# Performance work log

Hardware: AMD Instinct MI355X
Metric: run time of the kernel (lower is better)

Reference implementation:

```python
import jax, jax.numpy as jnp
import numpy as np

EMB = 768
N_HEADS = 12
HEAD_DIM = EMB // N_HEADS
EPS = 1e-5


def _gelu_tanh(x):
    c = jnp.sqrt(jnp.asarray(2.0 / jnp.pi, x.dtype))
    return 0.5 * x * (1.0 + jnp.tanh(c * (x + 0.044715 * x ** 3)))


def _layernorm(x, scale, shift):
    mean = jnp.mean(x, axis=-1, keepdims=True)
    var = jnp.mean((x - mean) ** 2, axis=-1, keepdims=True)
    return (x - mean) / jnp.sqrt(var + EPS) * scale + shift


def setup_inputs() -> dict:
    key = jax.random.key(0)
    ks = jax.random.split(key, 8)
    s = 0.02  # GPT-2 style init scale
    x = jax.random.normal(ks[0], (8, 1024, EMB), dtype=jnp.float32)
    # torch Linear weights are (out, in); no biases (qkv_bias=False everywhere)
    wq = jax.random.normal(ks[1], (EMB, EMB), dtype=jnp.float32) * s
    wk = jax.random.normal(ks[2], (EMB, EMB), dtype=jnp.float32) * s
    wv = jax.random.normal(ks[3], (EMB, EMB), dtype=jnp.float32) * s
    wo = jax.random.normal(ks[4], (EMB, EMB), dtype=jnp.float32) * s
    w1 = jax.random.normal(ks[5], (4 * EMB, EMB), dtype=jnp.float32) * s
    w2 = jax.random.normal(ks[6], (EMB, 4 * EMB), dtype=jnp.float32) * s
    ln1_scale = jnp.ones((EMB,), jnp.float32)
    ln1_shift = jnp.zeros((EMB,), jnp.float32)
    ln2_scale = jnp.ones((EMB,), jnp.float32)
    ln2_shift = jnp.zeros((EMB,), jnp.float32)
    return dict(x=x, wq=wq, wk=wk, wv=wv, wo=wo, w1=w1, w2=w2,
                ln1_scale=ln1_scale, ln1_shift=ln1_shift,
                ln2_scale=ln2_scale, ln2_shift=ln2_shift)


def reference(x, wq, wk, wv, wo, w1, w2, ln1_scale, ln1_shift, ln2_scale, ln2_shift):
    B, T, E = x.shape
    # --- attention sublayer (pre-LN) ---
    h = _layernorm(x, ln1_scale, ln1_shift)
    q = (h @ wq.T).reshape(B, T, N_HEADS, HEAD_DIM).transpose(0, 2, 1, 3)
    k = (h @ wk.T).reshape(B, T, N_HEADS, HEAD_DIM).transpose(0, 2, 1, 3)
    v = (h @ wv.T).reshape(B, T, N_HEADS, HEAD_DIM).transpose(0, 2, 1, 3)
    scores = jnp.einsum('bhqd,bhkd->bhqk', q, k)  # [B,H,T,T]
    causal = jnp.tril(jnp.ones((T, T), dtype=bool))
    scores = jnp.where(causal, scores, -jnp.inf)
    attn = jax.nn.softmax(scores / np.sqrt(HEAD_DIM), axis=-1)
    ctx = jnp.einsum('bhqk,bhkd->bhqd', attn, v)
    ctx = ctx.transpose(0, 2, 1, 3).reshape(B, T, E)
    x = x + ctx @ wo.T
    # --- FFN sublayer (pre-LN) ---
    h = _layernorm(x, ln2_scale, ln2_shift)
    h = _gelu_tanh(h @ w1.T) @ w2.T
    return x + h
```

## Files before the change

kernel.cpp:

```cpp
#include <hip/hip_runtime.h>
#include <hip/hip_bf16.h>
#include <cstdint>

#define EMB    768
#define NHEADS 12
#define HDIM   64
#define SEQ    1024
#define BATCH  8
#define MROWS  (BATCH*SEQ)
#define FFN    3072
#define W2E    (EMB*EMB)
#define W4E    (FFN*EMB)

typedef __bf16 bf16_t;
typedef bf16_t bf16x8 __attribute__((ext_vector_type(8)));
typedef float  f32x4  __attribute__((ext_vector_type(4)));

__device__ __forceinline__ float b2f(unsigned short u) {
    union { unsigned int i; float f; } t; t.i = ((unsigned int)u) << 16; return t.f;
}
__device__ __forceinline__ unsigned short f2b(float f) {
    union { float f; unsigned int i; } t; t.f = f;
    unsigned int lsb = (t.i >> 16) & 1u;
    t.i += 0x7fffu + lsb;
    return (unsigned short)(t.i >> 16);
}
__device__ __forceinline__ float gelu_f(float x) {
    float u = 0.7978845608028654f * (x + 0.044715f * x * x * x);
    return x * (1.f / (1.f + __expf(-2.f * u)));
}

#if defined(__has_builtin)
#if __has_builtin(__builtin_amdgcn_global_load_lds)
#define HAS_GLL 1
#endif
#endif
#ifndef HAS_GLL
#define HAS_GLL 0
#endif

__device__ __forceinline__ void gll16(const unsigned short* g, unsigned short* lds_wave_base) {
#if HAS_GLL
    __builtin_amdgcn_global_load_lds(
        (const __attribute__((address_space(1))) unsigned int*)g,
        (__attribute__((address_space(3))) unsigned int*)lds_wave_base, 16, 0, 0);
#endif
}

__device__ __forceinline__ int4 load8(const void* src, size_t eoff, bool f32) {
    if (f32) {
        const float4* p = reinterpret_cast<const float4*>((const float*)src + eoff);
        float4 a = p[0], b = p[1];
        union { unsigned short u[8]; int4 v; } r;
        r.u[0] = f2b(a.x); r.u[1] = f2b(a.y); r.u[2] = f2b(a.z); r.u[3] = f2b(a.w);
        r.u[4] = f2b(b.x); r.u[5] = f2b(b.y); r.u[6] = f2b(b.z); r.u[7] = f2b(b.w);
        return r.v;
    }
    return *reinterpret_cast<const int4*>((const unsigned short*)src + eoff);
}
__device__ __forceinline__ float4 load4f(const void* src, size_t eoff, bool f32) {
    if (f32) return *reinterpret_cast<const float4*>((const float*)src + eoff);
    ushort4 u = *reinterpret_cast<const ushort4*>((const unsigned short*)src + eoff);
    float4 r; r.x = b2f(u.x); r.y = b2f(u.y); r.z = b2f(u.z); r.w = b2f(u.w);
    return r;
}

struct DetectArgs { const unsigned short* p[11]; int n[11]; };

__global__ __launch_bounds__(256) void detect_all(DetectArgs a, int* __restrict__ flags) {
    __shared__ int cnt;
    if (threadIdx.x == 0) cnt = 0;
    __syncthreads();
    const unsigned short* src = a.p[blockIdx.x];
    int npairs = a.n[blockIdx.x] / 2;
    if (npairs > 4096) npairs = 4096;
    int local = 0;
    for (int p = threadIdx.x; p < npairs; p += 256) {
        unsigned short u0 = src[2 * p], u1 = src[2 * p + 1];
        int e0 = (u0 >> 7) & 0xFF;
        bool insane0 = (e0 == 0xFF) || (u0 != 0 && (e0 < 96 || e0 > 159));
        bool zpat    = (u0 == 0 && u1 != 0);
        if (insane0 || zpat) ++local;
    }
    atomicAdd(&cnt, local);
    __syncthreads();
    if (threadIdx.x == 0) flags[blockIdx.x] = (cnt * 8 > npairs) ? 1 : 0;
}

__global__ __launch_bounds__(256) void cvt_adapt(
        const void* __restrict__ src, unsigned short* __restrict__ dst,
        int n, const int* __restrict__ flag) {
    int i = blockIdx.x * 256 + threadIdx.x;
    if (i * 4 >= n) return;
    if (*flag) {
        float4 f = reinterpret_cast<const float4*>(src)[i];
        ushort4 o;
        o.x = f2b(f.x); o.y = f2b(f.y); o.z = f2b(f.z); o.w = f2b(f.w);
        reinterpret_cast<ushort4*>(dst)[i] = o;
    } else {
        reinterpret_cast<ushort4*>(dst)[i] = reinterpret_cast<const ushort4*>(src)[i];
    }
}

struct CvtArgs {
    const void* src[6];
    unsigned short* dst[6];
    int n[6];
    int blkoff[7];
    const int* F;
    int fidx[6];
};
__global__ __launch_bounds__(256) void cvt_weights(CvtArgs a) {
    int b = blockIdx.x, seg = 0;
    #pragma unroll
    for (int s = 0; s < 6; ++s) if (b >= a.blkoff[s + 1]) seg = s + 1;
    int i = (b - a.blkoff[seg]) * 256 + threadIdx.x;
    if (i * 4 >= a.n[seg]) return;
    if (a.F[a.fidx[seg]]) {
        float4 f = reinterpret_cast<const float4*>(a.src[seg])[i];
        ushort4 o;
        o.x = f2b(f.x); o.y = f2b(f.y); o.z = f2b(f.z); o.w = f2b(f.w);
        reinterpret_cast<ushort4*>(a.dst[seg])[i] = o;
    } else {
        reinterpret_cast<ushort4*>(a.dst[seg])[i] =
            reinterpret_cast<const ushort4*>(a.src[seg])[i];
    }
}

__global__ __launch_bounds__(256) void reduce2_kernel(
        const float* __restrict__ P, const unsigned short* __restrict__ resid,
        float* __restrict__ out, int n4) {
    int i = blockIdx.x * 256 + threadIdx.x;
    if (i >= n4) return;
    float4 a = reinterpret_cast<const float4*>(P)[i];
    float4 b = reinterpret_cast<const float4*>(P + (size_t)MROWS * EMB)[i];
    ushort4 r = reinterpret_cast<const ushort4*>(resid)[i];
    float4 o;
    o.x = a.x + b.x + b2f(r.x);
    o.y = a.y + b.y + b2f(r.y);
    o.z = a.z + b.z + b2f(r.z);
    o.w = a.w + b.w + b2f(r.w);
    reinterpret_cast<float4*>(out)[i] = o;
}

__global__ __launch_bounds__(256) void ln_kernel(
        const void* __restrict__ x,     const int* __restrict__ fx,
        const void* __restrict__ scale, const int* __restrict__ fsc,
        const void* __restrict__ shift, const int* __restrict__ fsh,
        unsigned short* __restrict__ out) {
    const bool xf = fx && *fx, scf = fsc && *fsc, shf = fsh && *fsh;
    int wave = threadIdx.x >> 6;
    int lane = threadIdx.x & 63;
    int row  = blockIdx.x * 4 + wave;
    const size_t rbase = (size_t)row * EMB;
    float v[12];
    float s = 0.f, s2 = 0.f;
    #pragma unroll
    for (int i = 0; i < 3; ++i) {
        float4 a = load4f(x, rbase + i * 256 + lane * 4, xf);
        v[i*4+0] = a.x; v[i*4+1] = a.y; v[i*4+2] = a.z; v[i*4+3] = a.w;
        s  += a.x + a.y + a.z + a.w;
        s2 += a.x*a.x + a.y*a.y + a.z*a.z + a.w*a.w;
    }
    #pragma unroll
    for (int off = 1; off < 64; off <<= 1) {
        s  += __shfl_xor(s,  off);
        s2 += __shfl_xor(s2, off);
    }
    float mean = s * (1.f / EMB);
    float var  = fmaxf(s2 * (1.f / EMB) - mean * mean, 0.f);
    float rstd = rsqrtf(var + 1e-5f);
    unsigned short* orow = out + rbase;
    #pragma unroll
    for (int i = 0; i < 3; ++i) {
        float4 sc = load4f(scale, i * 256 + lane * 4, scf);
        float4 sh = load4f(shift, i * 256 + lane * 4, shf);
        ushort4 o;
        o.x = f2b((v[i*4+0] - mean) * rstd * sc.x + sh.x);
        o.y = f2b((v[i*4+1] - mean) * rstd * sc.y + sh.y);
        o.z = f2b((v[i*4+2] - mean) * rstd * sc.z + sh.z);
        o.w = f2b((v[i*4+3] - mean) * rstd * sc.w + sh.w);
        *reinterpret_cast<ushort4*>(orow + i * 256 + lane * 4) = o;
    }
}

template<bool GELU, bool RESID, bool OUTF32>
__global__ __launch_bounds__(256) void gemm_lds(
        const unsigned short* __restrict__ A,
        const unsigned short* __restrict__ W,
        const void* R, const int* __restrict__ fR, size_t rOff,
        void* C, int M, int N, int K, int lda, int ldw) {
    constexpr int BK = 32;
    __shared__ __align__(16) unsigned short sA[128 * BK];
    __shared__ __align__(16) unsigned short sB[128 * BK];
    const int m0 = blockIdx.x * 128, n0 = blockIdx.y * 128;
    const int kz = blockIdx.z;
    const int t = threadIdx.x, wave = t >> 6, lane = t & 63;
    const int wrow = (wave >> 1) * 64, wcol = (wave & 1) * 64;
    const int quad = lane >> 4, lr = lane & 15;
    const int r0 = t >> 2;
    const int scg = (t & 3) ^ ((t >> 3) & 3);
    const int c0 = scg * 8;
    const int xq = quad ^ ((lr >> 1) & 3);
    const bool rf = fR && *fR;

    A += (size_t)kz * K;
    W += (size_t)kz * K;

    f32x4 acc[4][4];
    #pragma unroll
    for (int i = 0; i < 4; ++i)
        #pragma unroll
        for (int j = 0; j < 4; ++j)
            acc[i][j] = (f32x4){0.f, 0.f, 0.f, 0.f};

    const unsigned short* gA0 = A + (size_t)(m0 + r0) * lda + c0;
    const unsigned short* gA1 = A + (size_t)(m0 + 64 + r0) * lda + c0;
    const unsigned short* gB0 = W + (size_t)(n0 + r0) * ldw + c0;
    const unsigned short* gB1 = W + (size_t)(n0 + 64 + r0) * ldw + c0;
    unsigned short* lA0 = sA + wave * 512;
    unsigned short* lA1 = sA + 2048 + wave * 512;
    unsigned short* lB0 = sB + wave * 512;
    unsigned short* lB1 = sB + 2048 + wave * 512;

    for (int k0 = 0; k0 < K; k0 += BK) {
#if HAS_GLL
        gll16(gA0 + k0, lA0);
        gll16(gA1 + k0, lA1);
        gll16(gB0 + k0, lB0);
        gll16(gB1 + k0, lB1);
#else
        *reinterpret_cast<int4*>(sA + t * 8)        = *reinterpret_cast<const int4*>(gA0 + k0);
        *reinterpret_cast<int4*>(sA + 2048 + t * 8) = *reinterpret_cast<const int4*>(gA1 + k0);
        *reinterpret_cast<int4*>(sB + t * 8)        = *reinterpret_cast<const int4*>(gB0 + k0);
        *reinterpret_cast<int4*>(sB + 2048 + t * 8) = *reinterpret_cast<const int4*>(gB1 + k0);
#endif
        __syncthreads();
        bf16x8 af[4], bfv[4];
        #pragma unroll
        for (int i = 0; i < 4; ++i)
            af[i] = *reinterpret_cast<const bf16x8*>(
                sA + (wrow >> 6) * 2048 + (i * 16 + lr) * 32 + xq * 8);
        #pragma unroll
        for (int j = 0; j < 4; ++j)
            bfv[j] = *reinterpret_cast<const bf16x8*>(
                sB + (wcol >> 6) * 2048 + (j * 16 + lr) * 32 + xq * 8);
        #pragma unroll
        for (int i = 0; i < 4; ++i)
            #pragma unroll
            for (int j = 0; j < 4; ++j)
                acc[i][j] = __builtin_amdgcn_mfma_f32_16x16x32_bf16(af[i], bfv[j], acc[i][j], 0, 0, 0);
        __syncthreads();
    }

    float* Cf = (float*)C + (size_t)kz * M * N;
    #pragma unroll
    for (int i = 0; i < 4; ++i) {
        #pragma unroll
        for (int j = 0; j < 4; ++j) {
            #pragma unroll
            for (int r = 0; r < 4; ++r) {
                int row = m0 + wrow + i * 16 + quad * 4 + r;
                int col = n0 + wcol + j * 16 + lr;
                float val = acc[i][j][r];
                if (GELU) val = gelu_f(val);
                size_t idx = (size_t)row * N + col;
                if (RESID) {
                    float rv = rf ? ((const float*)R)[idx + rOff]
                                  : b2f(((const unsigned short*)R)[idx + rOff]);
                    val += rv;
                }
                if (OUTF32) Cf[idx] = val;
                else        ((unsigned short*)C)[idx] = f2b(val);
            }
        }
    }
}

template<bool GELU, bool RESID, bool OUTF32>
__global__ __launch_bounds__(256) void gemm_bt(
        const unsigned short* __restrict__ A,
        const void* __restrict__ W, const int* __restrict__ fW,
        const void* R, const int* __restrict__ fR, size_t rOff,
        void* C,
        int M, int N, int K) {
    const bool wf = fW && *fW;
    const bool rf = fR && *fR;
    constexpr int BK = 32, PAD = 8, LDW = BK + PAD;
    __shared__ __align__(16) unsigned short sA[128 * LDW];
    __shared__ __align__(16) unsigned short sB[128 * LDW];
    const int m0 = blockIdx.x * 128;
    const int n0 = blockIdx.y * 128;
    const int t    = threadIdx.x;
    const int wave = t >> 6, lane = t & 63;
    const int wrow = (wave >> 1) * 64, wcol = (wave & 1) * 64;
    const int quad = lane >> 4, lr = lane & 15;
    const int srow = t >> 2, scol = (t & 3) * 8;

    f32x4 acc[4][4];
    #pragma unroll
    for (int i = 0; i < 4; ++i)
        #pragma unroll
        for (int j = 0; j < 4; ++j)
            acc[i][j] = (f32x4){0.f, 0.f, 0.f, 0.f};

    const size_t aBase = (size_t)(m0 + srow) * K + scol;
    const size_t bBase = (size_t)(n0 + srow) * K + scol;

    for (int k0 = 0; k0 < K; k0 += BK) {
        int4 av0 = *reinterpret_cast<const int4*>(A + aBase + k0);
        int4 av1 = *reinterpret_cast<const int4*>(A + aBase + (size_t)64 * K + k0);
        int4 bv0 = load8(W, bBase + k0, wf);
        int4 bv1 = load8(W, bBase + (size_t)64 * K + k0, wf);
        *reinterpret_cast<int4*>(sA + srow * LDW + scol)        = av0;
        *reinterpret_cast<int4*>(sA + (srow + 64) * LDW + scol) = av1;
        *reinterpret_cast<int4*>(sB + srow * LDW + scol)        = bv0;
        *reinterpret_cast<int4*>(sB + (srow + 64) * LDW + scol) = bv1;
        __syncthreads();
        bf16x8 af[4], bfv[4];
        #pragma unroll
        for (int i = 0; i < 4; ++i)
            af[i] = *reinterpret_cast<const bf16x8*>(sA + (wrow + i * 16 + lr) * LDW + quad * 8);
        #pragma unroll
        for (int j = 0; j < 4; ++j)
            bfv[j] = *reinterpret_cast<const bf16x8*>(sB + (wcol + j * 16 + lr) * LDW + quad * 8);
        #pragma unroll
        for (int i = 0; i < 4; ++i)
            #pragma unroll
            for (int j = 0; j < 4; ++j)
                acc[i][j] = __builtin_amdgcn_mfma_f32_16x16x32_bf16(af[i], bfv[j], acc[i][j], 0, 0, 0);
        __syncthreads();
    }

    #pragma unroll
    for (int i = 0; i < 4; ++i) {
        #pragma unroll
        for (int j = 0; j < 4; ++j) {
            #pragma unroll
            for (int r = 0; r < 4; ++r) {
                int row = m0 + wrow + i * 16 + quad * 4 + r;
                int col = n0 + wcol + j * 16 + lr;
                float val = acc[i][j][r];
                if (GELU) val = gelu_f(val);
                size_t idx = (size_t)row * N + col;
                if (RESID) {
                    float rv = rf ? ((const float*)R)[idx + rOff]
                                  : b2f(((const unsigned short*)R)[idx + rOff]);
                    val += rv;
                }
                if (OUTF32) ((float*)C)[idx] = val;
                else        ((unsigned short*)C)[idx] = f2b(val);
            }
        }
    }
}

__global__ __launch_bounds__(256) void fattn_kernel(
        const unsigned short* __restrict__ q,
        const unsigned short* __restrict__ k,
        const unsigned short* __restrict__ v,
        int rs, unsigned short* __restrict__ ctx) {
    constexpr int VTP = 72;
    __shared__ unsigned short Vt[64 * VTP];
    __shared__ unsigned short Pl[4][16 * VTP];
    const int tid  = threadIdx.x;
    const int wave = tid >> 6, lane = tid & 63;
    const int quad = lane >> 4, lr = lane & 15;
    const int NH   = gridDim.x >> 3;
    const int head = blockIdx.x % NH;
    const int pr   = blockIdx.x / NH;
    const int bb   = head / NHEADS, hd = head % NHEADS;
    const size_t seqbase = (size_t)bb * SEQ;

    #pragma unroll
    for (int seg = 0; seg < 2; ++seg) {
        const int qt = seg == 0 ? (15 - pr) : pr;
        const int q0 = qt * 64 + wave * 16;

        bf16x8 aQ0, aQ1;
        {
            const unsigned short* qp = q + (seqbase + q0 + lr) * rs + hd * HDIM + quad * 8;
            aQ0 = *reinterpret_cast<const bf16x8*>(qp);
            aQ1 = *reinterpret_cast<const bf16x8*>(qp + 32);
        }

        f32x4 O[4];
        #pragma unroll
        for (int i = 0; i < 4; ++i) O[i] = (f32x4){0.f, 0.f, 0.f, 0.f};
        float mrow[4], lrow[4];
        #pragma unroll
        for (int r = 0; r < 4; ++r) { mrow[r] = -__builtin_inff(); lrow[r] = 0.f; }

        for (int kt = 0; kt <= qt; ++kt) {
            {
                const int vrow = tid >> 2;
                const int vcol = (tid & 3) * 16;
                const unsigned short* vp = v + (seqbase + kt * 64 + vrow) * rs + hd * HDIM + vcol;
                union { int4 v4; unsigned short u[8]; } ua, ub;
                ua.v4 = *reinterpret_cast<const int4*>(vp);
                ub.v4 = *reinterpret_cast<const int4*>(vp + 8);
                #pragma unroll
                for (int e = 0; e < 8; ++e) Vt[(vcol + e) * VTP + vrow]     = ua.u[e];
                #pragma unroll
                for (int e = 0; e < 8; ++e) Vt[(vcol + 8 + e) * VTP + vrow] = ub.u[e];
            }
            __syncthreads();

            f32x4 S[4];
            #pragma unroll
            for (int sub = 0; sub < 4; ++sub) {
                const unsigned short* kp = k + (seqbase + kt * 64 + sub * 16 + lr) * rs + hd * HDIM + quad * 8;
                bf16x8 b0 = *reinterpret_cast<const bf16x8*>(kp);
                bf16x8 b1 = *reinterpret_cast<const bf16x8*>(kp + 32);
                f32x4 accS = (f32x4){0.f, 0.f, 0.f, 0.f};
                accS = __builtin_amdgcn_mfma_f32_16x16x32_bf16(aQ0, b0, accS, 0, 0, 0);
                accS = __builtin_amdgcn_mfma_f32_16x16x32_bf16(aQ1, b1, accS, 0, 0, 0);
                S[sub] = accS;
            }
            const bool diag = (kt == qt);
            #pragma unroll
            for (int sub = 0; sub < 4; ++sub) {
                const int kg = kt * 64 + sub * 16 + lr;
                #pragma unroll
                for (int r = 0; r < 4; ++r) {
                    float s = S[sub][r] * 0.125f;
                    if (diag && kg > q0 + quad * 4 + r) s = -__builtin_inff();
                    S[sub][r] = s;
                }
            }
            float mnew[4], alpha[4];
            #pragma unroll
            for (int r = 0; r < 4; ++r) {
                float mx = fmaxf(fmaxf(S[0][r], S[1][r]), fmaxf(S[2][r], S[3][r]));
                #pragma unroll
                for (int m = 1; m < 16; m <<= 1) mx = fmaxf(mx, __shfl_xor(mx, m));
                mnew[r]  = fmaxf(mrow[r], mx);
                alpha[r] = __expf(mrow[r] - mnew[r]);
                mrow[r]  = mnew[r];
            }
            float rsum[4] = {0.f, 0.f, 0.f, 0.f};
            #pragma unroll
            for (int sub = 0; sub < 4; ++sub)
                #pragma unroll
                for (int r = 0; r < 4; ++r) {
                    float p = __expf(S[sub][r] - mnew[r]);
                    S[sub][r] = p;
                    rsum[r] += p;
                }
            #pragma unroll
            for (int r = 0; r < 4; ++r) {
                float rs2 = rsum[r];
                #pragma unroll
                for (int m = 1; m < 16; m <<= 1) rs2 += __shfl_xor(rs2, m);
                lrow[r] = lrow[r] * alpha[r] + rs2;
            }
            #pragma unroll
            for (int d = 0; d < 4; ++d)
                #pragma unroll
                for (int r = 0; r < 4; ++r)
                    O[d][r] *= alpha[r];

            unsigned short* Pw = Pl[wave];
            #pragma unroll
            for (int sub = 0; sub < 4; ++sub)
                #pragma unroll
                for (int r = 0; r < 4; ++r)
                    Pw[(quad * 4 + r) * VTP + sub * 16 + lr] = f2b(S[sub][r]);
            __syncthreads();

            #pragma unroll
            for (int c = 0; c < 2; ++c) {
                bf16x8 aP = *reinterpret_cast<const bf16x8*>(&Pw[lr * VTP + c * 32 + quad * 8]);
                #pragma unroll
                for (int d = 0; d < 4; ++d) {
                    bf16x8 bV = *reinterpret_cast<const bf16x8*>(&Vt[(d * 16 + lr) * VTP + c * 32 + quad * 8]);
                    O[d] = __builtin_amdgcn_mfma_f32_16x16x32_bf16(aP, bV, O[d], 0, 0, 0);
                }
            }
            __syncthreads();
        }

        #pragma unroll
        for (int r = 0; r < 4; ++r) {
            const float rinv = 1.f / lrow[r];
            const int qg = q0 + quad * 4 + r;
            unsigned short* crow = ctx + (seqbase + qg) * EMB + hd * HDIM;
            #pragma unroll
            for (int d = 0; d < 4; ++d)
                crow[d * 16 + lr] = f2b(O[d][r] * rinv);
        }
    }
}

extern "C" void kernel_launch(void* const* d_in, const int* in_sizes, int n_in,
                              void* d_out, int out_size, void* d_ws, size_t ws_size,
                              hipStream_t stream) {
    const void* x  = d_in[0];
    const void* wq = d_in[1], *wk = d_in[2], *wv = d_in[3], *wo = d_in[4];
    const void* w1 = d_in[5], *w2 = d_in[6];
    const void* g1 = d_in[7], *s1 = d_in[8], *g2 = d_in[9], *s2 = d_in[10];
    char* ws = (char*)d_ws;
    dim3 blk(256);

    int* F = (int*)ws;
    {
        DetectArgs da;
        for (int i = 0; i < 11; ++i) { da.p[i] = (const unsigned short*)d_in[i]; da.n[i] = in_sizes[i]; }
        detect_all<<<11, blk, 0, stream>>>(da, F);
    }

    const size_t SZE = (size_t)MROWS * EMB;
    const size_t SZB = SZE * 2;
    unsigned short* base = (unsigned short*)(ws + 256);
    dim3 g768(MROWS / 128, EMB / 128);

    const size_t FULLB = 256 + 2ULL * (2 * W4E) + 2ULL * (4 * W2E)
                       + 2ULL * ((size_t)MROWS * 2304) + 2 * SZB
                       + 2ULL * ((size_t)MROWS * FFN);
    const size_t FULLB2 = FULLB + 2ULL * SZE * 4;

    if (ws_size >= FULLB2) {
        unsigned short* w1b   = base;
        unsigned short* w2b   = w1b + W4E;
        unsigned short* wqkvb = w2b + W4E;
        unsigned short* wob   = wqkvb + 3 * W2E;
        unsigned short* P     = wob + W2E;
        unsigned short* B0    = P + (size_t)MROWS * 2304;
        unsigned short* B1    = B0 + SZE;
        unsigned short* G     = B1 + SZE;
        float*          PK    = (float*)(G + (size_t)MROWS * FFN);

        {
            CvtArgs ca;
            ca.src[0] = wq; ca.src[1] = wk; ca.src[2] = wv;
            ca.src[3] = wo; ca.src[4] = w1; ca.src[5] = w2;
            ca.dst[0] = wqkvb; ca.dst[1] = wqkvb + W2E; ca.dst[2] = wqkvb + 2 * W2E;
            ca.dst[3] = wob;   ca.dst[4] = w1b;         ca.dst[5] = w2b;
            ca.n[0] = ca.n[1] = ca.n[2] = ca.n[3] = W2E; ca.n[4] = ca.n[5] = W4E;
            int off = 0;
            for (int s = 0; s < 6; ++s) { ca.blkoff[s] = off; off += ca.n[s] / 1024; }
            ca.blkoff[6] = off;
            ca.F = F;
            ca.fidx[0] = 1; ca.fidx[1] = 2; ca.fidx[2] = 3;
            ca.fidx[3] = 4; ca.fidx[4] = 5; ca.fidx[5] = 6;
            cvt_weights<<<off, blk, 0, stream>>>(ca);
        }

        ln_kernel<<<MROWS / 4, blk, 0, stream>>>(x, F+0, g1, F+7, s1, F+8, B1);
        dim3 gqkv(MROWS / 128, 2304 / 128);
        gemm_lds<false, false, false><<<gqkv, blk, 0, stream>>>(B1, wqkvb, nullptr, nullptr, 0, P, MROWS, 2304, EMB, EMB, EMB);
        fattn_kernel<<<BATCH * NHEADS * 8, blk, 0, stream>>>(P, P + 768, P + 1536, 2304, B0);
        gemm_lds<false, true, false><<<g768, blk, 0, stream>>>(B0, wob, x, F+0, 0, B1, MROWS, EMB, EMB, EMB, EMB);
        ln_kernel<<<MROWS / 4, blk, 0, stream>>>(B1, nullptr, g2, F+9, s2, F+10, B0);
        dim3 gffn1(MROWS / 128, FFN / 128);
        gemm_lds<true, false, false><<<gffn1, blk, 0, stream>>>(B0, w1b, nullptr, nullptr, 0, G, MROWS, FFN, EMB, EMB, EMB);
        dim3 gsk(MROWS / 128, EMB / 128, 2);
        gemm_lds<false, false, true><<<gsk, blk, 0, stream>>>(G, w2b, nullptr, nullptr, 0, PK, MROWS, EMB, FFN / 2, FFN, FFN);
        reduce2_kernel<<<(SZE / 4 + 255) / 256, blk, 0, stream>>>(PK, B1, (float*)d_out, SZE / 4);
    } else if (ws_size >= FULLB) {
        unsigned short* w1b   = base;
        unsigned short* w2b   = w1b + W4E;
        unsigned short* wqkvb = w2b + W4E;
        unsigned short* wob   = wqkvb + 3 * W2E;
        unsigned short* P     = wob + W2E;
        unsigned short* B0    = P + (size_t)MROWS * 2304;
        unsigned short* B1    = B0 + SZE;
        unsigned short* G     = B1 + SZE;

        {
            CvtArgs ca;
            ca.src[0] = wq; ca.src[1] = wk; ca.src[2] = wv;
            ca.src[3] = wo; ca.src[4] = w1; ca.src[5] = w2;
            ca.dst[0] = wqkvb; ca.dst[1] = wqkvb + W2E; ca.dst[2] = wqkvb + 2 * W2E;
            ca.dst[3] = wob;   ca.dst[4] = w1b;         ca.dst[5] = w2b;
            ca.n[0] = ca.n[1] = ca.n[2] = ca.n[3] = W2E; ca.n[4] = ca.n[5] = W4E;
            int off = 0;
            for (int s = 0; s < 6; ++s) { ca.blkoff[s] = off; off += ca.n[s] / 1024; }
            ca.blkoff[6] = off;
            ca.F = F;
            ca.fidx[0] = 1; ca.fidx[1] = 2; ca.fidx[2] = 3;
            ca.fidx[3] = 4; ca.fidx[4] = 5; ca.fidx[5] = 6;
            cvt_weights<<<off, blk, 0, stream>>>(ca);
        }

        ln_kernel<<<MROWS / 4, blk, 0, stream>>>(x, F+0, g1, F+7, s1, F+8, B1);
        dim3 gqkv(MROWS / 128, 2304 / 128);
        gemm_lds<false, false, false><<<gqkv, blk, 0, stream>>>(B1, wqkvb, nullptr, nullptr, 0, P, MROWS, 2304, EMB, EMB, EMB);
        fattn_kernel<<<BATCH * NHEADS * 8, blk, 0, stream>>>(P, P + 768, P + 1536, 2304, B0);
        gemm_lds<false, true, false><<<g768, blk, 0, stream>>>(B0, wob, x, F+0, 0, B1, MROWS, EMB, EMB, EMB, EMB);
        ln_kernel<<<MROWS / 4, blk, 0, stream>>>(B1, nullptr, g2, F+9, s2, F+10, B0);
        dim3 gffn1(MROWS / 128, FFN / 128);
        gemm_lds<true, false, false><<<gffn1, blk, 0, stream>>>(B0, w1b, nullptr, nullptr, 0, G, MROWS, FFN, EMB, EMB, EMB);
        gemm_lds<false, true, true><<<g768, blk, 0, stream>>>(G, w2b, B1, nullptr, 0, d_out, MROWS, EMB, FFN, FFN, FFN);
    } else if (ws_size >= 256 + 4 * SZB) {
        unsigned short* B0 = base;
        unsigned short* B1 = B0 + SZE;
        unsigned short* B2 = B1 + SZE;
        unsigned short* B3 = B2 + SZE;
        ln_kernel<<<MROWS / 4, blk, 0, stream>>>(x, F+0, g1, F+7, s1, F+8, B0);
        gemm_bt<false, false, false><<<g768, blk, 0, stream>>>(B0, wq, F+1, nullptr, nullptr, 0, B1, MROWS, EMB, EMB);
        gemm_bt<false, false, false><<<g768, blk, 0, stream>>>(B0, wk, F+2, nullptr, nullptr, 0, B2, MROWS, EMB, EMB);
        gemm_bt<false, false, false><<<g768, blk, 0, stream>>>(B0, wv, F+3, nullptr, nullptr, 0, B3, MROWS, EMB, EMB);
        fattn_kernel<<<BATCH * NHEADS * 8, blk, 0, stream>>>(B1, B2, B3, EMB, B0);
        gemm_bt<false, true, false><<<g768, blk, 0, stream>>>(B0, wo, F+4, x, F+0, 0, B1, MROWS, EMB, EMB);
        ln_kernel<<<MROWS / 4, blk, 0, stream>>>(B1, nullptr, g2, F+9, s2, F+10, B2);
        dim3 c3072(2048 / 128, FFN / 128), c768(2048 / 128, EMB / 128);
        for (int c = 0; c < 4; ++c) {
            const size_t r0 = (size_t)c * 2048;
            gemm_bt<true, false, false><<<c3072, blk, 0, stream>>>(B2 + r0 * EMB, w1, F+5, nullptr, nullptr, 0, B3, 2048, FFN, EMB);
            gemm_bt<false, true, true><<<c768, blk, 0, stream>>>(B3, w2, F+6, B1 + r0 * EMB, nullptr, 0, (float*)d_out + r0 * EMB, 2048, EMB, FFN);
        }
    } else {
        unsigned short* hlow = (unsigned short*)d_out;
        unsigned short* x2up = (unsigned short*)d_out + SZE;
        unsigned short* wsQ = base;
        unsigned short* wsK = wsQ + (size_t)1024 * EMB;
        unsigned short* wsV = wsK + (size_t)1024 * EMB;
        unsigned short* wsC = wsV + (size_t)1024 * EMB;
        ln_kernel<<<MROWS / 4, blk, 0, stream>>>(x, F+0, g1, F+7, s1, F+8, hlow);
        dim3 q768(1024 / 128, EMB / 128);
        for (int grp = 0; grp < BATCH; ++grp) {
            const size_t r0 = (size_t)grp * 1024;
            gemm_bt<false, false, false><<<q768, blk, 0, stream>>>(hlow + r0 * EMB, wq, F+1, nullptr, nullptr, 0, wsQ, 1024, EMB, EMB);
            gemm_bt<false, false, false><<<q768, blk, 0, stream>>>(hlow + r0 * EMB, wk, F+2, nullptr, nullptr, 0, wsK, 1024, EMB, EMB);
            gemm_bt<false, false, false><<<q768, blk, 0, stream>>>(hlow + r0 * EMB, wv, F+3, nullptr, nullptr, 0, wsV, 1024, EMB, EMB);
            fattn_kernel<<<1 * NHEADS * 8, blk, 0, stream>>>(wsQ, wsK, wsV, EMB, wsC);
            gemm_bt<false, true, false><<<q768, blk, 0, stream>>>(wsC, wo, F+4, x, F+0, r0 * EMB, x2up + r0 * EMB, 1024, EMB, EMB);
        }
        unsigned short* xb = base;
        unsigned short* h2 = xb + (size_t)1024 * EMB;
        unsigned short* gb = h2 + (size_t)1024 * EMB;
        dim3 f3072(1024 / 128, FFN / 128), f768(1024 / 128, EMB / 128);
        for (int c = 0; c < BATCH; ++c) {
            const size_t r0 = (size_t)c * 1024;
            hipMemcpyAsync(xb, x2up + r0 * EMB, (size_t)1024 * EMB * 2,
                           hipMemcpyDeviceToDevice, stream);
            ln_kernel<<<1024 / 4, blk, 0, stream>>>(xb, nullptr, g2, F+9, s2, F+10, h2);
            gemm_bt<true, false, false><<<f3072, blk, 0, stream>>>(h2, w1, F+5, nullptr, nullptr, 0, gb, 1024, FFN, EMB);
            gemm_bt<false, true, true><<<f768, blk, 0, stream>>>(gb, w2, F+6, xb, nullptr, 0, (float*)d_out + r0 * EMB, 1024, EMB, FFN);
        }
    }
}
```

Before: 433.1 us.

## Double-buffer K/V tiles in LDS with swizzles and exp2 softmax in flash attention

The attention kernel now stages K tiles into LDS with global_load_lds and double-buffers K and transposed V, prefetching the next tile while the current one is computed. This drops one of the per-iteration block barriers. XOR swizzles on the K, V and P LDS layouts are meant to cut bank conflicts, and softmax uses exp2 with a prescaled log2e factor instead of __expf. It uses more LDS per block, which may lower occupancy, and the swizzle index arithmetic has to be right in every read and write.

```diff
diff --git a/kernel.cpp b/kernel.cpp
--- a/kernel.cpp
+++ b/kernel.cpp
@@ -29,6 +29,17 @@
     float u = 0.7978845608028654f * (x + 0.044715f * x * x * x);
     return x * (1.f / (1.f + __expf(-2.f * u)));
 }
+__device__ __forceinline__ float fexp2(float x) {
+#if defined(__has_builtin)
+#if __has_builtin(__builtin_amdgcn_exp2f)
+    return __builtin_amdgcn_exp2f(x);
+#else
+    return exp2f(x);
+#endif
+#else
+    return exp2f(x);
+#endif
+}
 
 #if defined(__has_builtin)
 #if __has_builtin(__builtin_amdgcn_global_load_lds)
@@ -44,6 +55,15 @@
     __builtin_amdgcn_global_load_lds(
         (const __attribute__((address_space(1))) unsigned int*)g,
         (__attribute__((address_space(3))) unsigned int*)lds_wave_base, 16, 0, 0);
+#endif
+}
+__device__ __forceinline__ void stage16(const unsigned short* g, unsigned short* lds_wave_base, int lane) {
+#if HAS_GLL
+    __builtin_amdgcn_global_load_lds(
+        (const __attribute__((address_space(1))) unsigned int*)g,
+        (__attribute__((address_space(3))) unsigned int*)lds_wave_base, 16, 0, 0);
+#else
+    *reinterpret_cast<int4*>(lds_wave_base + lane * 8) = *reinterpret_cast<const int4*>(g);
 #endif
 }
 
@@ -361,8 +381,9 @@
         const unsigned short* __restrict__ v,
         int rs, unsigned short* __restrict__ ctx) {
     constexpr int VTP = 72;
-    __shared__ unsigned short Vt[64 * VTP];
-    __shared__ unsigned short Pl[4][16 * VTP];
+    __shared__ __align__(16) unsigned short sK[2][64 * 64];
+    __shared__ __align__(16) unsigned short Vt[2][64 * VTP];
+    __shared__ __align__(16) unsigned short Pl[4][16 * VTP];
     const int tid  = threadIdx.x;
     const int wave = tid >> 6, lane = tid & 63;
     const int quad = lane >> 4, lr = lane & 15;
@@ -371,6 +392,16 @@
     const int pr   = blockIdx.x / NH;
     const int bb   = head / NHEADS, hd = head % NHEADS;
     const size_t seqbase = (size_t)bb * SEQ;
+    constexpr float C2 = 0.18033688011112042f;
+
+    const int krow0 = tid >> 3;
+    const int dreal = ((tid & 7) * 8) ^ ((krow0 & 7) << 3);
+    const int vrow = tid >> 2;
+    const int vcol = (tid & 3) * 16;
+    const int vxr  = vrow ^ ((tid & 3) << 4);
+    const int kswz = (lr & 7) << 3;
+    const int pswr = ((lr >> 2) & 3) << 3;
+    unsigned short* Pw = Pl[wave];
 
     #pragma unroll
     for (int seg = 0; seg < 2; ++seg) {
@@ -391,27 +422,41 @@
         #pragma unroll
         for (int r = 0; r < 4; ++r) { mrow[r] = -__builtin_inff(); lrow[r] = 0.f; }
 
+        {
+            const unsigned short* kp = k + (seqbase + krow0) * rs + hd * HDIM + dreal;
+            stage16(kp,                   &sK[0][wave * 512],        lane);
+            stage16(kp + (size_t)32 * rs, &sK[0][2048 + wave * 512], lane);
+            const unsigned short* vp = v + (seqbase + vrow) * rs + hd * HDIM + vcol;
+            union { int4 v4; unsigned short u[8]; } pa, pb;
+            pa.v4 = *reinterpret_cast<const int4*>(vp);
+            pb.v4 = *reinterpret_cast<const int4*>(vp + 8);
+            #pragma unroll
+            for (int e = 0; e < 8; ++e) Vt[0][(vcol + e) * VTP + vxr]     = pa.u[e];
+            #pragma unroll
+            for (int e = 0; e < 8; ++e) Vt[0][(vcol + 8 + e) * VTP + vxr] = pb.u[e];
+        }
+        __syncthreads();
+
         for (int kt = 0; kt <= qt; ++kt) {
-            {
-                const int vrow = tid >> 2;
-                const int vcol = (tid & 3) * 16;
-                const unsigned short* vp = v + (seqbase + kt * 64 + vrow) * rs + hd * HDIM + vcol;
-                union { int4 v4; unsigned short u[8]; } ua, ub;
+            const int b = kt & 1;
+            union { int4 v4; unsigned short u[8]; } ua, ub;
+            if (kt < qt) {
+                const unsigned short* kp = k + (seqbase + (size_t)(kt + 1) * 64 + krow0) * rs
+                                         + hd * HDIM + dreal;
+                stage16(kp,                   &sK[b ^ 1][wave * 512],        lane);
+                stage16(kp + (size_t)32 * rs, &sK[b ^ 1][2048 + wave * 512], lane);
+                const unsigned short* vp = v + (seqbase + (size_t)(kt + 1) * 64 + vrow) * rs
+                                         + hd * HDIM + vcol;
                 ua.v4 = *reinterpret_cast<const int4*>(vp);
                 ub.v4 = *reinterpret_cast<const int4*>(vp + 8);
-                #pragma unroll
-                for (int e = 0; e < 8; ++e) Vt[(vcol + e) * VTP + vrow]     = ua.u[e];
-                #pragma unroll
-                for (int e = 0; e < 8; ++e) Vt[(vcol + 8 + e) * VTP + vrow] = ub.u[e];
-            }
-            __syncthreads();
+            }
 
             f32x4 S[4];
             #pragma unroll
             for (int sub = 0; sub < 4; ++sub) {
-                const unsigned short* kp = k + (seqbase + kt * 64 + sub * 16 + lr) * rs + hd * HDIM + quad * 8;
-                bf16x8 b0 = *reinterpret_cast<const bf16x8*>(kp);
-                bf16x8 b1 = *reinterpret_cast<const bf16x8*>(kp + 32);
+                const unsigned short* kr = &sK[b][(sub * 16 + lr) * 64];
+                bf16x8 b0 = *reinterpret_cast<const bf16x8*>(kr + ((quad * 8) ^ kswz));
+                bf16x8 b1 = *reinterpret_cast<const bf16x8*>(kr + ((32 + quad * 8) ^ kswz));
                 f32x4 accS = (f32x4){0.f, 0.f, 0.f, 0.f};
                 accS = __builtin_amdgcn_mfma_f32_16x16x32_bf16(aQ0, b0, accS, 0, 0, 0);
                 accS = __builtin_amdgcn_mfma_f32_16x16x32_bf16(aQ1, b1, accS, 0, 0, 0);
@@ -423,7 +468,7 @@
                 const int kg = kt * 64 + sub * 16 + lr;
                 #pragma unroll
                 for (int r = 0; r < 4; ++r) {
-                    float s = S[sub][r] * 0.125f;
+                    float s = S[sub][r] * C2;
                     if (diag && kg > q0 + quad * 4 + r) s = -__builtin_inff();
                     S[sub][r] = s;
                 }
@@ -435,7 +480,7 @@
                 #pragma unroll
                 for (int m = 1; m < 16; m <<= 1) mx = fmaxf(mx, __shfl_xor(mx, m));
                 mnew[r]  = fmaxf(mrow[r], mx);
-                alpha[r] = __expf(mrow[r] - mnew[r]);
+                alpha[r] = fexp2(mrow[r] - mnew[r]);
                 mrow[r]  = mnew[r];
             }
             float rsum[4] = {0.f, 0.f, 0.f, 0.f};
@@ -443,7 +488,7 @@
             for (int sub = 0; sub < 4; ++sub)
                 #pragma unroll
                 for (int r = 0; r < 4; ++r) {
-                    float p = __expf(S[sub][r] - mnew[r]);
+                    float p = fexp2(S[sub][r] - mnew[r]);
                     S[sub][r] = p;
                     rsum[r] += p;
                 }
@@ -454,26 +499,35 @@
                 for (int m = 1; m < 16; m <<= 1) rs2 += __shfl_xor(rs2, m);
                 lrow[r] = lrow[r] * alpha[r] + rs2;
             }
+
+            #pragma unroll
+            for (int sub = 0; sub < 4; ++sub)
+                #pragma unroll
+                for (int r = 0; r < 4; ++r) {
+                    bf16_t hv = (bf16_t)S[sub][r];
+                    Pw[(quad * 4 + r) * VTP + ((sub * 16 + lr) ^ (quad << 3))] =
+                        *reinterpret_cast<unsigned short*>(&hv);
+                }
+            if (kt < qt) {
+                #pragma unroll
+                for (int e = 0; e < 8; ++e) Vt[b ^ 1][(vcol + e) * VTP + vxr]     = ua.u[e];
+                #pragma unroll
+                for (int e = 0; e < 8; ++e) Vt[b ^ 1][(vcol + 8 + e) * VTP + vxr] = ub.u[e];
+            }
             #pragma unroll
             for (int d = 0; d < 4; ++d)
                 #pragma unroll
                 for (int r = 0; r < 4; ++r)
                     O[d][r] *= alpha[r];
 
-            unsigned short* Pw = Pl[wave];
-            #pragma unroll
-            for (int sub = 0; sub < 4; ++sub)
-                #pragma unroll
-                for (int r = 0; r < 4; ++r)
-                    Pw[(quad * 4 + r) * VTP + sub * 16 + lr] = f2b(S[sub][r]);
-            __syncthreads();
-
             #pragma unroll
             for (int c = 0; c < 2; ++c) {
-                bf16x8 aP = *reinterpret_cast<const bf16x8*>(&Pw[lr * VTP + c * 32 + quad * 8]);
+                bf16x8 aP = *reinterpret_cast<const bf16x8*>(
+                    &Pw[lr * VTP + ((c * 32 + quad * 8) ^ pswr)]);
                 #pragma unroll
                 for (int d = 0; d < 4; ++d) {
-                    bf16x8 bV = *reinterpret_cast<const bf16x8*>(&Vt[(d * 16 + lr) * VTP + c * 32 + quad * 8]);
+                    bf16x8 bV = *reinterpret_cast<const bf16x8*>(
+                        &Vt[b][(d * 16 + lr) * VTP + ((c * 32 + quad * 8) ^ (d << 4))]);
                     O[d] = __builtin_amdgcn_mfma_f32_16x16x32_bf16(aP, bV, O[d], 0, 0, 0);
                 }
             }
```

New measurement: 402.3 us. 7.1% less time.
